# Kernel optimization log

Hardware: AMD Instinct MI355X
Metric: run time of the kernel (lower is better)

The kernel has to match this reference:

```python
import jax, jax.numpy as jnp
import numpy as np

B, C, H, W = 4, 64, 96, 96
O = 64          # out_channel
K = 9           # 3x3 kernel positions
PAD = 1


def conv3x3(x, w, b):
    # NCHW 3x3 conv, stride 1, pad 1
    y = jax.lax.conv_general_dilated(
        x, w, window_strides=(1, 1), padding=((PAD, PAD), (PAD, PAD)),
        dimension_numbers=("NCHW", "OIHW", "NCHW"))
    return y + b[None, :, None, None]


def deform_conv3x3(x, offset, w, b):
    """torchvision-style DeformConv2d, 3x3, stride 1, pad 1, 1 offset group.
    x: [B, Cin, H, W]; offset: [B, 2*K, H, W] ordered (dy, dx) per kernel pos.
    """
    Bb, Cin, Hh, Ww = x.shape
    off = offset.reshape(Bb, K, 2, Hh, Ww)
    ky, kx = jnp.meshgrid(jnp.arange(3), jnp.arange(3), indexing="ij")
    ky = ky.reshape(K).astype(x.dtype)
    kx = kx.reshape(K).astype(x.dtype)
    hh = jnp.arange(Hh, dtype=x.dtype)
    ww = jnp.arange(Ww, dtype=x.dtype)
    # sampling coords: p0 + p_k + delta_p  -> [B, K, H, W]
    py = hh[None, None, :, None] - PAD + ky[None, :, None, None] + off[:, :, 0]
    px = ww[None, None, None, :] - PAD + kx[None, :, None, None] + off[:, :, 1]

    y0 = jnp.floor(py).astype(jnp.int32)
    x0 = jnp.floor(px).astype(jnp.int32)
    dy = py - y0.astype(x.dtype)
    dx = px - x0.astype(x.dtype)

    x_flat = x.reshape(Bb, Cin, Hh * Ww)

    def gather(yi, xi, wgt):
        valid = ((yi >= 0) & (yi < Hh) & (xi >= 0) & (xi < Ww)).astype(x.dtype)
        idx = (jnp.clip(yi, 0, Hh - 1) * Ww + jnp.clip(xi, 0, Ww - 1)).reshape(Bb, -1)
        vals = jax.vmap(lambda xf, ix: xf[:, ix])(x_flat, idx)  # [B, Cin, K*H*W]
        return vals * (wgt * valid).reshape(Bb, 1, -1)

    sampled = (gather(y0,     x0,     (1 - dy) * (1 - dx))
             + gather(y0,     x0 + 1, (1 - dy) * dx)
             + gather(y0 + 1, x0,     dy * (1 - dx))
             + gather(y0 + 1, x0 + 1, dy * dx))
    sampled = sampled.reshape(Bb, Cin, K, Hh, Ww)
    out = jnp.einsum("bckhw,ock->bohw", sampled, w.reshape(O, Cin, K))
    return out + b[None, :, None, None]


def setup_inputs() -> dict:
    key = jax.random.key(0)
    ks = jax.random.split(key, 6)
    ref_feat = jax.random.normal(ks[0], (B, C, H, W), dtype=jnp.float32)
    dist_feat = jax.random.normal(ks[1], (B, C, H, W), dtype=jnp.float32)
    offset_w = jax.random.normal(ks[2], (2 * K, C, 3, 3), dtype=jnp.float32) * 0.01
    offset_b = jnp.zeros((2 * K,), dtype=jnp.float32)
    deform_w = jax.random.normal(ks[3], (O, 3 * C, 3, 3), dtype=jnp.float32) * 0.05
    deform_b = jax.random.normal(ks[4], (O,), dtype=jnp.float32) * 0.05
    return {"ref_feat": ref_feat, "dist_feat": dist_feat,
            "offset_w": offset_w, "offset_b": offset_b,
            "deform_w": deform_w, "deform_b": deform_b}


def reference(ref_feat, dist_feat, offset_w, offset_b, deform_w, deform_b):
    offset = conv3x3(ref_feat, offset_w, offset_b)
    diff = (ref_feat - dist_feat) ** 2
    feat_in = jnp.concatenate((ref_feat, dist_feat, diff), axis=1)  # [B, 3C, H, W]
    feat = deform_conv3x3(feat_in, offset, deform_w, deform_b)
    feat = jax.nn.relu(feat)
    return (feat, diff)
```

## Files before the change

kernel.cpp:

```cpp
#include <hip/hip_runtime.h>
#include <hip/hip_fp16.h>

#define Wd    96
#define Hd    96
#define HW    9216
#define Bn    4
#define Cn    64
#define C3    192
#define On    64
#define NPIX  (Bn*HW)
#define NFEAT (Bn*Cn*HW)
#define NWTB  (9*6*4*512)
#define NWTB2 (18*2*64*8)
#define NRB3  (Bn*(HW/32))

#define HR2   6
#define HC    21
#define HPITCH 400
#define NPR2  (HR2*HC)
#define SELEM (NPR2*24)
#define HALO_B (NPR2*HPITCH)
#define REDA_B (2*2*64*9*4)
#define NFBLK 1152

typedef __attribute__((ext_vector_type(8))) short s8v;
typedef __attribute__((ext_vector_type(8))) _Float16 h8v;
typedef __attribute__((ext_vector_type(4))) unsigned int u4v;
typedef __attribute__((ext_vector_type(4))) float f4v;

__device__ __forceinline__ unsigned packh(float lo, float hi) {
    __half2 h = __floats2half2_rn(lo, hi);
    return __builtin_bit_cast(unsigned, h);
}

__global__ __launch_bounds__(256) void repack_wts_kernel(
        const float* __restrict__ ref,
        const float* __restrict__ dist,
        unsigned int* __restrict__ packed,
        float* __restrict__ out_diff,
        const float* __restrict__ dw,
        const float* __restrict__ ow,
        __half* __restrict__ wtb,
        __half* __restrict__ wtb2) {
    __shared__ unsigned lds[96][33];

    int tid = threadIdx.x;

    if (blockIdx.x >= NRB3) {
        int e = (int)(blockIdx.x - NRB3) * 256 + tid;
        if (e < NWTB) {
            int j = e & 7;
            int L = (e >> 3) & 63;
            int mt = (e >> 9) & 3;
            int rest = e >> 11;
            int kc = rest % 6;
            int tap = rest / 6;
            int o = mt * 16 + (L & 15);
            int c = kc * 32 + (L >> 4) * 8 + j;
            wtb[e] = __float2half(dw[((size_t)o * C3 + c) * 9 + tap]);
        } else if (e < NWTB + NWTB2) {
            int e2 = e - NWTB;
            int j = e2 & 7;
            int L = (e2 >> 3) & 63;
            int mt = (e2 >> 9) & 1;
            int kc2 = e2 >> 10;
            int v = mt * 16 + (L & 15);
            int k = kc2 * 32 + ((L >> 4) & 3) * 8 + j;
            int c = k & 63;
            int tap = k >> 6;
            float val = (v < 18) ? ow[((size_t)v * Cn + c) * 9 + tap] : 0.f;
            wtb2[e2] = __float2half(val);
        }
        return;
    }

    int blk = blockIdx.x;
    int b = blk / (HW / 32);
    int pb = (blk - b * (HW / 32)) * 32;
    int pxg = tid & 7;
    int chp = tid >> 3;

    size_t base0 = ((size_t)(b * Cn + 2 * chp)) * HW + pb + pxg * 4;
    size_t base1 = base0 + HW;

    f4v r0 = *(const f4v*)(ref + base0);
    f4v r1 = *(const f4v*)(ref + base1);
    f4v d0 = *(const f4v*)(dist + base0);
    f4v d1 = *(const f4v*)(dist + base1);

    f4v q0 = (r0 - d0) * (r0 - d0);
    f4v q1 = (r1 - d1) * (r1 - d1);
    *(f4v*)(out_diff + base0) = q0;
    *(f4v*)(out_diff + base1) = q1;

#pragma unroll
    for (int j = 0; j < 4; ++j) {
        int p = pxg * 4 + j;
        lds[chp][p]      = packh(r0[j], r1[j]);
        lds[32 + chp][p] = packh(d0[j], d1[j]);
        lds[64 + chp][p] = packh(q0[j], q1[j]);
    }
    __syncthreads();

    unsigned* pko = packed + (size_t)(b * HW + pb) * 96;
#pragma unroll
    for (int k = 0; k < 12; ++k) {
        int i = tid + k * 256;
        int p = i / 96;
        int cp = i - p * 96;
        pko[p * 96 + cp] = lds[cp][p];
    }
}

struct Ctx {
    int o00, o01, o10, o11;
    int l00, l01, l10, l11;
    float W00, W01, W10, W11;
    int inh;
};

__device__ __forceinline__ Ctx mkctx(int t, int y, int x, int xb, int yb,
                                     float2 o2) {
    Ctx c;
    float py = (float)(y - 1 + t / 3) + o2.x;
    float pxs = (float)(x - 1 + t % 3) + o2.y;
    float fy = floorf(py), fx = floorf(pxs);
    int y0 = (int)fy, x0 = (int)fx;
    int y1 = y0 + 1, x1 = x0 + 1;
    float ay = py - fy, ax = pxs - fx;
    bool vy0 = (unsigned)y0 < (unsigned)Hd;
    bool vy1 = (unsigned)y1 < (unsigned)Hd;
    bool vx0 = (unsigned)x0 < (unsigned)Wd;
    bool vx1 = (unsigned)x1 < (unsigned)Wd;
    c.W00 = (vy0 && vx0) ? (1.f - ay) * (1.f - ax) : 0.f;
    c.W01 = (vy0 && vx1) ? (1.f - ay) * ax : 0.f;
    c.W10 = (vy1 && vx0) ? ay * (1.f - ax) : 0.f;
    c.W11 = (vy1 && vx1) ? ay * ax : 0.f;
    int y0c = min(max(y0, 0), Hd - 1), y1c = min(max(y1, 0), Hd - 1);
    int x0c = min(max(x0, 0), Wd - 1), x1c = min(max(x1, 0), Wd - 1);
    c.o00 = (y0c * Wd + x0c) * (C3 * 2);
    c.o01 = (y0c * Wd + x1c) * (C3 * 2);
    c.o10 = (y1c * Wd + x0c) * (C3 * 2);
    c.o11 = (y1c * Wd + x1c) * (C3 * 2);
    int iy0 = y0c - yb + 2, iy1 = y1c - yb + 2;
    int ix0 = x0c - xb + 3, ix1 = x1c - xb + 3;
    c.inh = ((unsigned)iy0 < (unsigned)HR2) & ((unsigned)iy1 < (unsigned)HR2) &
            ((unsigned)ix0 < (unsigned)HC) & ((unsigned)ix1 < (unsigned)HC);
    c.l00 = (iy0 * HC + ix0) * HPITCH;
    c.l01 = (iy0 * HC + ix1) * HPITCH;
    c.l10 = (iy1 * HC + ix0) * HPITCH;
    c.l11 = (iy1 * HC + ix1) * HPITCH;
    return c;
}

__device__ __forceinline__ __half2 uh2(unsigned u) {
    return __builtin_bit_cast(__half2, u);
}

__device__ __forceinline__ void bilin_mfma(const s8v* rw, const Ctx& cc,
        const s8v* __restrict__ Ap, int t, int kb, int L, f4v* acc) {
    __half2 w00 = __float2half2_rn(cc.W00);
    __half2 w01 = __float2half2_rn(cc.W01);
    __half2 w10 = __float2half2_rn(cc.W10);
    __half2 w11 = __float2half2_rn(cc.W11);
#pragma unroll
    for (int i = 0; i < 3; ++i) {
        int kc = kb + i;
        u4v u00 = __builtin_bit_cast(u4v, rw[0 * 3 + i]);
        u4v u01 = __builtin_bit_cast(u4v, rw[1 * 3 + i]);
        u4v u10 = __builtin_bit_cast(u4v, rw[2 * 3 + i]);
        u4v u11 = __builtin_bit_cast(u4v, rw[3 * 3 + i]);
        u4v bu;
#pragma unroll
        for (int p = 0; p < 4; ++p) {
            __half2 v = __hmul2(uh2(u00[p]), w00);
            v = __hfma2(uh2(u01[p]), w01, v);
            v = __hfma2(uh2(u10[p]), w10, v);
            v = __hfma2(uh2(u11[p]), w11, v);
            bu[p] = __builtin_bit_cast(unsigned, v);
        }
        h8v bfrag = __builtin_bit_cast(h8v, bu);
#pragma unroll
        for (int mt = 0; mt < 4; ++mt) {
            h8v a = __builtin_bit_cast(h8v, Ap[((t * 6 + kc) * 4 + mt) * 64 + L]);
            acc[mt] = __builtin_amdgcn_mfma_f32_16x16x32_f16(a, bfrag, acc[mt], 0, 0, 0);
        }
    }
}

__global__ __launch_bounds__(384, 3) void fused_mfma(
        const __half* __restrict__ packed,
        const __half* __restrict__ wtb2,
        const float* __restrict__ ob,
        const __half* __restrict__ wtb,
        const float* __restrict__ db,
        float* __restrict__ out) {
    __shared__ __align__(16) char smem[HALO_B + REDA_B + 2 * 16 * 18 * 4];
    f4v* halo = (f4v*)smem;
    float* redA = (float*)(smem + HALO_B);
    float (*off_l)[18] = (float(*)[18])(smem + HALO_B + REDA_B);
    float* redB = (float*)smem;

    int tid = threadIdx.x;
    int L = tid & 63;
    int wv = tid >> 6;
    int g  = wv / 3;
    int kv = wv - g * 3;
    int px = L & 15;
    int lg = L >> 4;
    int blk = blockIdx.x;
    int region = (blk & 7) * 144 + (blk >> 3);
    int b = region / 288;
    int rt = region - b * 288;
    int yt = rt / 6;
    int xt = rt - yt * 6;
    int yb = yt * 2, xb = xt * 16;
    int y = yb + g, x = xb + px;
    int pb = y * Wd + xb;
    int tbase = kv * 3;

    const char* pkb = (const char*)packed + (size_t)b * HW * (C3 * 2);
    const char* hb = (const char*)halo;

    {
        f4v stg[8];
        int slot[8];
#pragma unroll
        for (int k = 0; k < 8; ++k) {
            int i = tid + k * 384;
            bool act = (k < 7) ? true : (tid < SELEM - 7 * 384);
            int pr = i / 24, ck = i - pr * 24;
            int iy = pr / HC, ix = pr - iy * HC;
            int gy = min(max(yb - 2 + iy, 0), Hd - 1);
            int gx = min(max(xb - 3 + ix, 0), Wd - 1);
            slot[k] = act ? (pr * (HPITCH / 16) + ck) : -1;
            if (act)
                stg[k] = *(const f4v*)(pkb + ((size_t)(gy * Wd + gx)) * (C3 * 2) + ck * 16);
        }
#pragma unroll
        for (int k = 0; k < 8; ++k)
            if (slot[k] >= 0) halo[slot[k]] = stg[k];
    }
    __syncthreads();

    {
        const s8v* Ap = (const s8v*)wtb2;
        f4v acc0 = {0.f, 0.f, 0.f, 0.f};
        f4v acc1 = {0.f, 0.f, 0.f, 0.f};
#pragma unroll
        for (int tt = 0; tt < 3; ++tt) {
            int t = tbase + tt;
            int ty = t / 3, tx = t - ty * 3;
            int yy = y - 1 + ty, xx = x - 1 + tx;
            bool val = (unsigned)yy < (unsigned)Hd && (unsigned)xx < (unsigned)Wd;
            short m = val ? (short)-1 : (short)0;
            int lofs = ((g + 1 + ty) * HC + (px + 2 + tx)) * HPITCH + lg * 16;
#pragma unroll
            for (int kc = 0; kc < 2; ++kc) {
                s8v braw = *(const s8v*)(hb + lofs + kc * 64) & m;
                h8v bfrag = __builtin_bit_cast(h8v, braw);
                h8v a0 = __builtin_bit_cast(h8v, Ap[((t * 2 + kc) * 2 + 0) * 64 + L]);
                h8v a1 = __builtin_bit_cast(h8v, Ap[((t * 2 + kc) * 2 + 1) * 64 + L]);
                acc0 = __builtin_amdgcn_mfma_f32_16x16x32_f16(a0, bfrag, acc0, 0, 0, 0);
                acc1 = __builtin_amdgcn_mfma_f32_16x16x32_f16(a1, bfrag, acc1, 0, 0, 0);
            }
        }
        if (kv != 0) {
            float* r = redA + ((g * 2 + kv - 1) * 64 + L) * 9;
#pragma unroll
            for (int i = 0; i < 4; ++i) r[i] = acc0[i];
#pragma unroll
            for (int i = 0; i < 4; ++i) r[4 + i] = acc1[i];
        }
        __syncthreads();
        if (kv == 0) {
            const float* r0 = redA + ((g * 2 + 0) * 64 + L) * 9;
            const float* r1 = redA + ((g * 2 + 1) * 64 + L) * 9;
#pragma unroll
            for (int r = 0; r < 4; ++r) {
                int v = lg * 4 + r;
                off_l[g * 16 + px][v] = acc0[r] + r0[r] + r1[r] + ob[v];
            }
            if (lg == 0) {
#pragma unroll
                for (int r = 0; r < 2; ++r)
                    off_l[g * 16 + px][16 + r] = acc1[r] + r0[4 + r] + r1[4 + r] + ob[16 + r];
            }
        }
        __syncthreads();
    }

    const s8v* Ap = (const s8v*)wtb;

    Ctx ctx[3];
    int ok = 1;
#pragma unroll
    for (int tt = 0; tt < 3; ++tt) {
        int t = tbase + tt;
        float2 o2 = {off_l[g * 16 + px][2 * t], off_l[g * 16 + px][2 * t + 1]};
        ctx[tt] = mkctx(t, y, x, xb, yb, o2);
        ok &= ctx[tt].inh;
    }

    f4v acc[4];
    acc[0] = acc[1] = acc[2] = acc[3] = (f4v){0.f, 0.f, 0.f, 0.f};

    if (__all(ok)) {
#pragma unroll
        for (int h = 0; h < 6; ++h) {
            int tt = h >> 1;
            int t = tbase + tt;
            int kb = (h & 1) * 3;
            const Ctx cc = ctx[tt];
            s8v rw[12];
#pragma unroll
            for (int i = 0; i < 3; ++i) {
                int co = ((kb + i) * 4 + lg) * 16;
                rw[0 * 3 + i] = *(const s8v*)(hb + cc.l00 + co);
                rw[1 * 3 + i] = *(const s8v*)(hb + cc.l01 + co);
                rw[2 * 3 + i] = *(const s8v*)(hb + cc.l10 + co);
                rw[3 * 3 + i] = *(const s8v*)(hb + cc.l11 + co);
            }
            bilin_mfma(rw, cc, Ap, t, kb, L, acc);
        }
    } else {
#pragma unroll
        for (int h = 0; h < 6; ++h) {
            int tt = h >> 1;
            int t = tbase + tt;
            int kb = (h & 1) * 3;
            const Ctx cc = ctx[tt];
            s8v rw[12];
#pragma unroll
            for (int i = 0; i < 3; ++i) {
                int co = ((kb + i) * 4 + lg) * 16;
                rw[0 * 3 + i] = *(const s8v*)(pkb + cc.o00 + co);
                rw[1 * 3 + i] = *(const s8v*)(pkb + cc.o01 + co);
                rw[2 * 3 + i] = *(const s8v*)(pkb + cc.o10 + co);
                rw[3 * 3 + i] = *(const s8v*)(pkb + cc.o11 + co);
            }
            bilin_mfma(rw, cc, Ap, t, kb, L, acc);
        }
    }

    __syncthreads();
    if (kv != 0) {
        float* r = redB + ((g * 2 + kv - 1) * 64 + L) * 17;
#pragma unroll
        for (int mt = 0; mt < 4; ++mt)
#pragma unroll
            for (int q = 0; q < 4; ++q)
                r[mt * 4 + q] = acc[mt][q];
    }
    __syncthreads();
    if (kv == 0) {
        const float* r0 = redB + ((g * 2 + 0) * 64 + L) * 17;
        const float* r1 = redB + ((g * 2 + 1) * 64 + L) * 17;
#pragma unroll
        for (int mt = 0; mt < 4; ++mt) {
#pragma unroll
            for (int q = 0; q < 4; ++q) {
                int o = mt * 16 + lg * 4 + q;
                float v = acc[mt][q] + r0[mt * 4 + q] + r1[mt * 4 + q] + db[o];
                out[((size_t)(b * On + o)) * HW + pb + px] = fmaxf(v, 0.f);
            }
        }
    }
}

extern "C" void kernel_launch(void* const* d_in, const int* in_sizes, int n_in,
                              void* d_out, int out_size, void* d_ws, size_t ws_size,
                              hipStream_t stream) {
    const float* ref  = (const float*)d_in[0];
    const float* dist = (const float*)d_in[1];
    const float* ow   = (const float*)d_in[2];
    const float* ob   = (const float*)d_in[3];
    const float* dw   = (const float*)d_in[4];
    const float* db   = (const float*)d_in[5];

    float* out = (float*)d_out;

    __half* ws_wtb  = (__half*)d_ws;
    __half* ws_wtb2 = ws_wtb + NWTB;
    __half* ws_pk   = ws_wtb2 + NWTB2;

    int wts_blocks = (NWTB + NWTB2 + 255) / 256;
    repack_wts_kernel<<<NRB3 + wts_blocks, 256, 0, stream>>>(
        ref, dist, (unsigned int*)ws_pk, out + NFEAT, dw, ow, ws_wtb, ws_wtb2);
    fused_mfma<<<NFBLK, 384, 0, stream>>>(
        ws_pk, ws_wtb2, ob, ws_wtb, db, out);
}
```

Baseline: 119.2 us.

## Compute offset conv in one wave per row, drop LDS reduction, raise occupancy

The offset convolution is now computed entirely by the kv==0 wave of each row group over all 9 taps, instead of splitting the taps across three waves and reducing partial sums through an LDS buffer. This removes the redA shared buffer and one barrier. The smaller LDS footprint lets launch bounds ask for 4 blocks per CU instead of 3. The repack kernel also writes packed output as 16-byte vector stores per pixel instead of scalar strided stores. In exchange, two of the three waves sit idle during the offset stage, which lengthens that stage's critical path.

```diff
diff --git a/kernel.cpp b/kernel.cpp
--- a/kernel.cpp
+++ b/kernel.cpp
@@ -20,7 +20,6 @@
 #define NPR2  (HR2*HC)
 #define SELEM (NPR2*24)
 #define HALO_B (NPR2*HPITCH)
-#define REDA_B (2*2*64*9*4)
 #define NFBLK 1152
 
 typedef __attribute__((ext_vector_type(8))) short s8v;
@@ -102,13 +101,18 @@
     }
     __syncthreads();
 
-    unsigned* pko = packed + (size_t)(b * HW + pb) * 96;
-#pragma unroll
-    for (int k = 0; k < 12; ++k) {
-        int i = tid + k * 256;
-        int p = i / 96;
-        int cp = i - p * 96;
-        pko[p * 96 + cp] = lds[cp][p];
+    {
+        int p = tid >> 3;
+        int part = tid & 7;
+        unsigned* pko = packed + ((size_t)(b * HW + pb) + p) * 96 + part * 12;
+#pragma unroll
+        for (int q = 0; q < 3; ++q) {
+            u4v w;
+#pragma unroll
+            for (int j = 0; j < 4; ++j)
+                w[j] = lds[part * 12 + q * 4 + j][p];
+            *(u4v*)(pko + q * 4) = w;
+        }
     }
 }
 
@@ -188,17 +192,16 @@
     }
 }
 
-__global__ __launch_bounds__(384, 3) void fused_mfma(
+__global__ __launch_bounds__(384, 4) void fused_mfma(
         const __half* __restrict__ packed,
         const __half* __restrict__ wtb2,
         const float* __restrict__ ob,
         const __half* __restrict__ wtb,
         const float* __restrict__ db,
         float* __restrict__ out) {
-    __shared__ __align__(16) char smem[HALO_B + REDA_B + 2 * 16 * 18 * 4];
+    __shared__ __align__(16) char smem[HALO_B + 2 * 16 * 18 * 4];
     f4v* halo = (f4v*)smem;
-    float* redA = (float*)(smem + HALO_B);
-    float (*off_l)[18] = (float(*)[18])(smem + HALO_B + REDA_B);
+    float (*off_l)[18] = (float(*)[18])(smem + HALO_B);
     float* redB = (float*)smem;
 
     int tid = threadIdx.x;
@@ -243,13 +246,12 @@
     }
     __syncthreads();
 
-    {
+    if (kv == 0) {
         const s8v* Ap = (const s8v*)wtb2;
         f4v acc0 = {0.f, 0.f, 0.f, 0.f};
         f4v acc1 = {0.f, 0.f, 0.f, 0.f};
 #pragma unroll
-        for (int tt = 0; tt < 3; ++tt) {
-            int t = tbase + tt;
+        for (int t = 0; t < 9; ++t) {
             int ty = t / 3, tx = t - ty * 3;
             int yy = y - 1 + ty, xx = x - 1 + tx;
             bool val = (unsigned)yy < (unsigned)Hd && (unsigned)xx < (unsigned)Wd;
@@ -265,30 +267,18 @@
                 acc1 = __builtin_amdgcn_mfma_f32_16x16x32_f16(a1, bfrag, acc1, 0, 0, 0);
             }
         }
-        if (kv != 0) {
-            float* r = redA + ((g * 2 + kv - 1) * 64 + L) * 9;
-#pragma unroll
-            for (int i = 0; i < 4; ++i) r[i] = acc0[i];
-#pragma unroll
-            for (int i = 0; i < 4; ++i) r[4 + i] = acc1[i];
-        }
-        __syncthreads();
-        if (kv == 0) {
-            const float* r0 = redA + ((g * 2 + 0) * 64 + L) * 9;
-            const float* r1 = redA + ((g * 2 + 1) * 64 + L) * 9;
-#pragma unroll
-            for (int r = 0; r < 4; ++r) {
-                int v = lg * 4 + r;
-                off_l[g * 16 + px][v] = acc0[r] + r0[r] + r1[r] + ob[v];
-            }
-            if (lg == 0) {
-#pragma unroll
-                for (int r = 0; r < 2; ++r)
-                    off_l[g * 16 + px][16 + r] = acc1[r] + r0[4 + r] + r1[4 + r] + ob[16 + r];
-            }
-        }
-        __syncthreads();
-    }
+#pragma unroll
+        for (int r = 0; r < 4; ++r) {
+            int v = lg * 4 + r;
+            off_l[g * 16 + px][v] = acc0[r] + ob[v];
+        }
+        if (lg == 0) {
+#pragma unroll
+            for (int r = 0; r < 2; ++r)
+                off_l[g * 16 + px][16 + r] = acc1[r] + ob[16 + r];
+        }
+    }
+    __syncthreads();
 
     const s8v* Ap = (const s8v*)wtb;
 
```

Result: faster. 116.0 us (-2.7%).
